# Optimization experiments

Measured on AMD Instinct MI355X. Metric: run time of the kernel, lower is better.

Reference implementation:

```python
import jax, jax.numpy as jnp
import numpy as np

EPS = 1e-6

def rms_norm(x, w):
    xf = x.astype(jnp.float32)
    xf = xf * jax.lax.rsqrt(jnp.mean(jnp.square(xf), axis=-1, keepdims=True) + EPS)
    return xf.astype(x.dtype) * w

def rotate_pairs(x):
    x = x.reshape(*x.shape[:-1], -1, 2)
    x1, x2 = x[..., 0], x[..., 1]
    return jnp.stack((-x2, x1), axis=-1).reshape(*x.shape[:-2], -1)

def apply_rope_axis(x, coords, inv_freq):
    # x: [B, H, T, axis_width]; coords: [T]; inv_freq: [axis_dim]
    angles = coords[:, None].astype(jnp.float32) * inv_freq[None, :]  # [T, axis_dim]
    cos = jnp.repeat(jnp.cos(angles), 2, axis=-1).astype(x.dtype)  # [T, axis_width]
    sin = jnp.repeat(jnp.sin(angles), 2, axis=-1).astype(x.dtype)
    return x * cos[None, None] + rotate_pairs(x) * sin[None, None]

def modulate(x, shift, scale):
    return x * (1.0 + scale[:, None, :]) + shift[:, None, :]

def setup_inputs() -> dict:
    key = jax.random.key(0)
    ks = jax.random.split(key, 16)
    B, T, D = 2, 2048, 1024
    HD = 64            # head_dim
    HID = 4096         # swiglu hidden (dim * mlp_ratio)
    CD = 1024          # cond_dim
    s = lambda n: 1.0 / np.sqrt(n)
    return {
        "x": jax.random.normal(ks[0], (B, T, D), jnp.float32),
        "cond": jax.random.normal(ks[1], (B, CD), jnp.float32),
        "norm1_w": jnp.ones((D,), jnp.float32),
        "qkv_w": jax.random.normal(ks[2], (3 * D, D), jnp.float32) * s(D),
        "q_norm_w": jnp.ones((HD,), jnp.float32),
        "k_norm_w": jnp.ones((HD,), jnp.float32),
        "proj_w": jax.random.normal(ks[3], (D, D), jnp.float32) * s(D),
        "proj_b": jnp.zeros((D,), jnp.float32),
        "norm2_w": jnp.ones((D,), jnp.float32),
        "fc1_w": jax.random.normal(ks[4], (2 * HID, D), jnp.float32) * s(D),
        "fc1_b": jnp.zeros((2 * HID,), jnp.float32),
        "fc2_w": jax.random.normal(ks[5], (D, HID), jnp.float32) * s(HID),
        "fc2_b": jnp.zeros((D,), jnp.float32),
        "ada_w": jax.random.normal(ks[6], (6 * D, CD), jnp.float32) * 0.02,
        "ada_b": jnp.zeros((6 * D,), jnp.float32),
        "height": 64,
        "width": 32,
    }

def reference(x, cond, norm1_w, qkv_w, q_norm_w, k_norm_w, proj_w, proj_b,
              norm2_w, fc1_w, fc1_b, fc2_w, fc2_b, ada_w, ada_b, height, width):
    B, T, D = x.shape
    HD = q_norm_w.shape[0]
    NH = D // HD
    scale = HD ** -0.5
    axis_dim = HD // 4
    axis_w = axis_dim * 2
    inv_freq = 1.0 / (10000.0 ** (jnp.arange(axis_dim, dtype=jnp.float32) / axis_dim))

    # AdaLN-Zero conditioning
    ada = jax.nn.silu(cond) @ ada_w.T + ada_b  # [B, 6D]
    sh_a, sc_a, g_a, sh_m, sc_m, g_m = jnp.split(ada, 6, axis=-1)

    # --- attention branch ---
    residual = x
    h = modulate(rms_norm(x, norm1_w), sh_a, sc_a)
    qkv = (h @ qkv_w.T).reshape(B, T, 3, NH, HD)
    q, k, v = qkv[:, :, 0], qkv[:, :, 1], qkv[:, :, 2]  # [B, T, NH, HD]
    q = rms_norm(q, q_norm_w)
    k = rms_norm(k, k_norm_w)
    q = q.transpose(0, 2, 1, 3)  # [B, NH, T, HD]
    k = k.transpose(0, 2, 1, 3)
    v = v.transpose(0, 2, 1, 3)

    # 2D RoPE: y coords on first axis_w dims, x coords on next axis_w dims
    yy, xx = jnp.meshgrid(jnp.arange(height), jnp.arange(width), indexing="ij")
    yy, xx = yy.reshape(-1), xx.reshape(-1)  # [T]
    q = jnp.concatenate([
        apply_rope_axis(q[..., :axis_w], yy, inv_freq),
        apply_rope_axis(q[..., axis_w:2 * axis_w], xx, inv_freq),
        q[..., 2 * axis_w:]], axis=-1)
    k = jnp.concatenate([
        apply_rope_axis(k[..., :axis_w], yy, inv_freq),
        apply_rope_axis(k[..., axis_w:2 * axis_w], xx, inv_freq),
        k[..., 2 * axis_w:]], axis=-1)

    attn = jax.nn.softmax(jnp.einsum("bhqd,bhkd->bhqk", q, k) * scale, axis=-1)
    h = jnp.einsum("bhqk,bhkd->bhqd", attn, v).transpose(0, 2, 1, 3).reshape(B, T, D)
    h = h @ proj_w.T + proj_b
    x = residual + g_a[:, None, :] * h

    # --- SwiGLU MLP branch ---
    residual = x
    h = modulate(rms_norm(x, norm2_w), sh_m, sc_m)
    value, gate = jnp.split(h @ fc1_w.T + fc1_b, 2, axis=-1)
    h = (value * jax.nn.silu(gate)) @ fc2_w.T + fc2_b
    return residual + g_m[:, None, :] * h
```

## Files before the change

kernel.cpp:

```cpp
#include <hip/hip_runtime.h>
#include <hip/hip_bf16.h>

#define B_   2
#define T_   2048
#define D_   1024
#define NH_  16
#define HD_  64
#define HID_ 4096
#define CD_  1024
#define SIX_D (6*D_)

typedef __bf16 bf16x8 __attribute__((ext_vector_type(8)));
typedef float  f32x4  __attribute__((ext_vector_type(4)));
typedef float  f32x16 __attribute__((ext_vector_type(16)));

__device__ __forceinline__ unsigned short f2bf(float f){
  union { float f; unsigned u; } v; v.f = f;
  unsigned r = v.u + 0x7FFFu + ((v.u >> 16) & 1u);
  return (unsigned short)(r >> 16);
}
__device__ __forceinline__ float bf2f(unsigned short u){
  union { unsigned x; float f; } v; v.x = ((unsigned)u) << 16; return v.f;
}

__device__ __forceinline__ void gl_lds16(const void* g, void* l){
  __builtin_amdgcn_global_load_lds(
      (__attribute__((address_space(1))) void*)const_cast<void*>(g),
      (__attribute__((address_space(3))) void*)l, 16, 0, 0);
}

__global__ void k_conv_all(const float* __restrict__ s0, const float* __restrict__ s1,
                           const float* __restrict__ s2, const float* __restrict__ s3,
                           unsigned short* __restrict__ d0, unsigned short* __restrict__ d1,
                           unsigned short* __restrict__ d2, unsigned short* __restrict__ d3){
  int bid = blockIdx.x;
  const float* s; unsigned short* d; int base;
  if (bid < 3072)      { s = s0; d = d0; base = bid; }
  else if (bid < 4096) { s = s1; d = d1; base = bid - 3072; }
  else if (bid < 12288){ s = s2; d = d2; base = bid - 4096; }
  else                 { s = s3; d = d3; base = bid - 12288; }
  int i = base*256 + threadIdx.x;
  float4 v = reinterpret_cast<const float4*>(s)[i];
  ushort4 o;
  o.x = f2bf(v.x); o.y = f2bf(v.y); o.z = f2bf(v.z); o.w = f2bf(v.w);
  reinterpret_cast<ushort4*>(d)[i] = o;
}

__global__ void k_ada(const float* __restrict__ cond, const float* __restrict__ ada_w,
                      const float* __restrict__ ada_b, float* __restrict__ ada){
  __shared__ float sc[CD_];
  __shared__ float part[4][64];
  int b = blockIdx.y;
  int tid = threadIdx.x;
  for (int i = tid; i < CD_; i += 256){
    float c = cond[b*CD_ + i];
    sc[i] = c / (1.f + __expf(-c));
  }
  __syncthreads();
  int col = blockIdx.x*64 + (tid & 63);
  int qk  = tid >> 6;
  const float* wr = ada_w + (size_t)col*CD_ + qk*256;
  const float* scq = sc + qk*256;
  float acc = 0.f;
  #pragma unroll 4
  for (int k = 0; k < 256; k++) acc += scq[k]*wr[k];
  part[qk][tid & 63] = acc;
  __syncthreads();
  if (tid < 64){
    float a = part[0][tid] + part[1][tid] + part[2][tid] + part[3][tid];
    int c = blockIdx.x*64 + tid;
    ada[b*SIX_D + c] = a + ada_b[c];
  }
}

__global__ void k_norm_mod(const float* __restrict__ x, const float* __restrict__ w,
                           const float* __restrict__ ada, int sh_off, int sc_off,
                           unsigned short* __restrict__ out){
  int row = blockIdx.x;
  int b = row >> 11;
  int tid = threadIdx.x;
  float4 xv = reinterpret_cast<const float4*>(x + (size_t)row*D_)[tid];
  float ss = xv.x*xv.x + xv.y*xv.y + xv.z*xv.z + xv.w*xv.w;
  #pragma unroll
  for (int m = 32; m > 0; m >>= 1) ss += __shfl_xor(ss, m, 64);
  __shared__ float red[4];
  int wave = tid >> 6;
  if ((tid & 63) == 0) red[wave] = ss;
  __syncthreads();
  float tot = red[0]+red[1]+red[2]+red[3];
  float rn = rsqrtf(tot * (1.f/(float)D_) + 1e-6f);
  float4 wv  = reinterpret_cast<const float4*>(w)[tid];
  float4 scv = reinterpret_cast<const float4*>(ada + b*SIX_D + sc_off)[tid];
  float4 shv = reinterpret_cast<const float4*>(ada + b*SIX_D + sh_off)[tid];
  ushort4 o;
  o.x = f2bf(xv.x*rn*wv.x*(1.f+scv.x)+shv.x);
  o.y = f2bf(xv.y*rn*wv.y*(1.f+scv.y)+shv.y);
  o.z = f2bf(xv.z*rn*wv.z*(1.f+scv.z)+shv.z);
  o.w = f2bf(xv.w*rn*wv.w*(1.f+scv.w)+shv.w);
  reinterpret_cast<ushort4*>(out + (size_t)row*D_)[tid] = o;
}

enum { EPI_F32 = 0, EPI_RESID = 1, EPI_BF16 = 2 };

template<int EPI>
__launch_bounds__(256)
__global__ void k_gemm_bt(const unsigned short* __restrict__ A,
                          const unsigned short* __restrict__ W,
                          int M, int N, int K,
                          void* __restrict__ outp,
                          const float* __restrict__ resid,
                          const float* __restrict__ ada, int g_off,
                          const float* __restrict__ bias){
  __shared__ __align__(16) unsigned short As[2][128*32];
  __shared__ __align__(16) unsigned short Bs[2][128*32];
  const int tid = threadIdx.x;
  const int wave = tid >> 6, lane = tid & 63;
  const int wm = (wave >> 1)*64, wn = (wave & 1)*64;
  const int m0 = blockIdx.y*128, n0 = blockIdx.x*128;
  const int fr = lane & 15, fq = lane >> 4;
  const int sl = (fq ^ ((fr >> 1) & 3))*8;
  const int r0 = tid >> 2, c0 = tid & 3;
  const int g0 = c0 ^ ((r0 >> 1) & 3);
  const int r1 = r0 + 64;
  const int g1 = c0 ^ ((r1 >> 1) & 3);
  const unsigned short* gA0 = A + (size_t)(m0 + r0)*K + g0*8;
  const unsigned short* gA1 = A + (size_t)(m0 + r1)*K + g1*8;
  const unsigned short* gB0 = W + (size_t)(n0 + r0)*K + g0*8;
  const unsigned short* gB1 = W + (size_t)(n0 + r1)*K + g1*8;
  const int l0 = (tid & ~63)*8, l1 = ((256 + tid) & ~63)*8;
  f32x4 acc[4][4] = {};
  auto stage = [&](int buf){
    gl_lds16(gA0, &As[buf][l0]);
    gl_lds16(gA1, &As[buf][l1]);
    gl_lds16(gB0, &Bs[buf][l0]);
    gl_lds16(gB1, &Bs[buf][l1]);
    gA0 += 32; gA1 += 32; gB0 += 32; gB1 += 32;
  };
  stage(0); stage(1);
  const int NK = K >> 5;
  for (int t = 0; t < NK; t++){
    const int cur = t & 1;
    if (t < NK - 1) asm volatile("s_waitcnt vmcnt(4)" ::: "memory");
    else            asm volatile("s_waitcnt vmcnt(0)" ::: "memory");
    __builtin_amdgcn_s_barrier();
    bf16x8 af[4], bfr[4];
    #pragma unroll
    for (int i = 0; i < 4; i++){
      af[i]  = *(const bf16x8*)&As[cur][(wm + i*16 + fr)*32 + sl];
      bfr[i] = *(const bf16x8*)&Bs[cur][(wn + i*16 + fr)*32 + sl];
    }
    __builtin_amdgcn_s_setprio(1);
    #pragma unroll
    for (int i = 0; i < 4; i++)
      #pragma unroll
      for (int j = 0; j < 4; j++)
        acc[i][j] = __builtin_amdgcn_mfma_f32_16x16x32_bf16(af[i], bfr[j], acc[i][j], 0,0,0);
    __builtin_amdgcn_s_setprio(0);
    __builtin_amdgcn_s_barrier();
    if (t + 2 < NK) stage(cur);
  }
  #pragma unroll
  for (int i = 0; i < 4; i++){
    #pragma unroll
    for (int j = 0; j < 4; j++){
      int col = n0 + wn + j*16 + fr;
      #pragma unroll
      for (int r = 0; r < 4; r++){
        int row = m0 + wm + i*16 + fq*4 + r;
        float v = acc[i][j][r];
        if (EPI == EPI_F32){
          ((float*)outp)[(size_t)row*N + col] = v;
        } else if (EPI == EPI_BF16){
          ((unsigned short*)outp)[(size_t)row*N + col] = f2bf(v);
        } else {
          int b = row >> 11;
          float g = ada[b*SIX_D + g_off + col];
          ((float*)outp)[(size_t)row*N + col] = resid[(size_t)row*N + col] + g*(v + bias[col]);
        }
      }
    }
  }
}

template<int EPI>
__launch_bounds__(256)
__global__ void k_gemm_bt64(const unsigned short* __restrict__ A,
                            const unsigned short* __restrict__ W,
                            int M, int N, int K,
                            void* __restrict__ outp,
                            const float* __restrict__ resid,
                            const float* __restrict__ ada, int g_off,
                            const float* __restrict__ bias){
  __shared__ __align__(16) unsigned short As[2][64*32];
  __shared__ __align__(16) unsigned short Bs[2][128*32];
  const int tid = threadIdx.x;
  const int wave = tid >> 6, lane = tid & 63;
  const int wm = (wave >> 1)*32, wn = (wave & 1)*64;
  const int m0 = blockIdx.y*64, n0 = blockIdx.x*128;
  const int fr = lane & 15, fq = lane >> 4;
  const int sl = (fq ^ ((fr >> 1) & 3))*8;
  const int r0 = tid >> 2, c0 = tid & 3;
  const int g0 = c0 ^ ((r0 >> 1) & 3);
  const int r1 = r0 + 64;
  const int g1 = c0 ^ ((r1 >> 1) & 3);
  const unsigned short* gA0 = A + (size_t)(m0 + r0)*K + g0*8;
  const unsigned short* gB0 = W + (size_t)(n0 + r0)*K + g0*8;
  const unsigned short* gB1 = W + (size_t)(n0 + r1)*K + g1*8;
  const int l0 = (tid & ~63)*8, l1 = ((256 + tid) & ~63)*8;
  f32x4 acc[2][4] = {};
  auto stage = [&](int buf){
    gl_lds16(gA0, &As[buf][l0]);
    gl_lds16(gB0, &Bs[buf][l0]);
    gl_lds16(gB1, &Bs[buf][l1]);
    gA0 += 32; gB0 += 32; gB1 += 32;
  };
  stage(0); stage(1);
  const int NK = K >> 5;
  for (int t = 0; t < NK; t++){
    const int cur = t & 1;
    if (t < NK - 1) asm volatile("s_waitcnt vmcnt(3)" ::: "memory");
    else            asm volatile("s_waitcnt vmcnt(0)" ::: "memory");
    __builtin_amdgcn_s_barrier();
    bf16x8 af[2], bfr[4];
    #pragma unroll
    for (int i = 0; i < 2; i++)
      af[i]  = *(const bf16x8*)&As[cur][(wm + i*16 + fr)*32 + sl];
    #pragma unroll
    for (int j = 0; j < 4; j++)
      bfr[j] = *(const bf16x8*)&Bs[cur][(wn + j*16 + fr)*32 + sl];
    __builtin_amdgcn_s_setprio(1);
    #pragma unroll
    for (int i = 0; i < 2; i++)
      #pragma unroll
      for (int j = 0; j < 4; j++)
        acc[i][j] = __builtin_amdgcn_mfma_f32_16x16x32_bf16(af[i], bfr[j], acc[i][j], 0,0,0);
    __builtin_amdgcn_s_setprio(0);
    __builtin_amdgcn_s_barrier();
    if (t + 2 < NK) stage(cur);
  }
  #pragma unroll
  for (int i = 0; i < 2; i++){
    #pragma unroll
    for (int j = 0; j < 4; j++){
      int col = n0 + wn + j*16 + fr;
      #pragma unroll
      for (int r = 0; r < 4; r++){
        int row = m0 + wm + i*16 + fq*4 + r;
        float v = acc[i][j][r];
        if (EPI == EPI_F32){
          ((float*)outp)[(size_t)row*N + col] = v;
        } else if (EPI == EPI_BF16){
          ((unsigned short*)outp)[(size_t)row*N + col] = f2bf(v);
        } else {
          int b = row >> 11;
          float g = ada[b*SIX_D + g_off + col];
          ((float*)outp)[(size_t)row*N + col] = resid[(size_t)row*N + col] + g*(v + bias[col]);
        }
      }
    }
  }
}

__launch_bounds__(256)
__global__ void k_gemm_fc1(const unsigned short* __restrict__ A,
                           const unsigned short* __restrict__ W,
                           const float* __restrict__ bias,
                           unsigned short* __restrict__ out){
  __shared__ __align__(16) unsigned short As[2][128*32];
  __shared__ __align__(16) unsigned short Bv[2][64*32];
  __shared__ __align__(16) unsigned short Bg[2][64*32];
  const int K = D_;
  const int tid = threadIdx.x;
  const int wave = tid >> 6, lane = tid & 63;
  const int wm = (wave >> 1)*64, wn = (wave & 1)*32;
  const int m0 = blockIdx.y*128, n0 = blockIdx.x*64;
  const int fr = lane & 15, fq = lane >> 4;
  const int sl = (fq ^ ((fr >> 1) & 3))*8;
  const int r0 = tid >> 2, c0 = tid & 3;
  const int g0 = c0 ^ ((r0 >> 1) & 3);
  const int r1 = r0 + 64;
  const int g1 = c0 ^ ((r1 >> 1) & 3);
  const unsigned short* gA0 = A + (size_t)(m0 + r0)*K + g0*8;
  const unsigned short* gA1 = A + (size_t)(m0 + r1)*K + g1*8;
  const unsigned short* gBv = W + (size_t)(n0 + r0)*K + g0*8;
  const unsigned short* gBg = W + (size_t)(HID_ + n0 + r0)*K + g0*8;
  const int l0 = (tid & ~63)*8, l1 = ((256 + tid) & ~63)*8;
  f32x4 accv[4][2] = {}, accg[4][2] = {};
  auto stage = [&](int buf){
    gl_lds16(gA0, &As[buf][l0]);
    gl_lds16(gA1, &As[buf][l1]);
    gl_lds16(gBv, &Bv[buf][l0]);
    gl_lds16(gBg, &Bg[buf][l0]);
    gA0 += 32; gA1 += 32; gBv += 32; gBg += 32;
  };
  stage(0); stage(1);
  const int NK = K >> 5;
  for (int t = 0; t < NK; t++){
    const int cur = t & 1;
    if (t < NK - 1) asm volatile("s_waitcnt vmcnt(4)" ::: "memory");
    else            asm volatile("s_waitcnt vmcnt(0)" ::: "memory");
    __builtin_amdgcn_s_barrier();
    bf16x8 af[4], bv[2], bg[2];
    #pragma unroll
    for (int i = 0; i < 4; i++)
      af[i] = *(const bf16x8*)&As[cur][(wm + i*16 + fr)*32 + sl];
    #pragma unroll
    for (int j = 0; j < 2; j++){
      bv[j] = *(const bf16x8*)&Bv[cur][(wn + j*16 + fr)*32 + sl];
      bg[j] = *(const bf16x8*)&Bg[cur][(wn + j*16 + fr)*32 + sl];
    }
    __builtin_amdgcn_s_setprio(1);
    #pragma unroll
    for (int i = 0; i < 4; i++)
      #pragma unroll
      for (int j = 0; j < 2; j++){
        accv[i][j] = __builtin_amdgcn_mfma_f32_16x16x32_bf16(af[i], bv[j], accv[i][j], 0,0,0);
        accg[i][j] = __builtin_amdgcn_mfma_f32_16x16x32_bf16(af[i], bg[j], accg[i][j], 0,0,0);
      }
    __builtin_amdgcn_s_setprio(0);
    __builtin_amdgcn_s_barrier();
    if (t + 2 < NK) stage(cur);
  }
  #pragma unroll
  for (int i = 0; i < 4; i++){
    #pragma unroll
    for (int j = 0; j < 2; j++){
      int col = n0 + wn + j*16 + fr;
      #pragma unroll
      for (int r = 0; r < 4; r++){
        int row = m0 + wm + i*16 + fq*4 + r;
        float vv = accv[i][j][r] + bias[col];
        float gg = accg[i][j][r] + bias[HID_ + col];
        float h = vv * (gg / (1.f + __expf(-gg)));
        out[(size_t)row*HID_ + col] = f2bf(h);
      }
    }
  }
}

__global__ void k_qkv_post(const unsigned short* __restrict__ qkv,
                           const float* __restrict__ qw, const float* __restrict__ kw,
                           const int* __restrict__ wptr,
                           unsigned short* __restrict__ q, unsigned short* __restrict__ k){
  int idx = blockIdx.x*4 + (threadIdx.x >> 6);
  int h = idx & (NH_-1);
  int t = (idx >> 4) & (T_-1);
  int b = idx >> 15;
  int d = threadIdx.x & 63;
  const unsigned short* base = qkv + (size_t)(b*T_ + t)*3072;
  float qv = bf2f(base[h*64 + d]);
  float kv = bf2f(base[1024 + h*64 + d]);
  float sq = qv*qv, sk = kv*kv;
  #pragma unroll
  for (int m = 32; m > 0; m >>= 1){ sq += __shfl_xor(sq, m, 64); sk += __shfl_xor(sk, m, 64); }
  qv *= rsqrtf(sq*(1.f/64.f) + 1e-6f) * qw[d];
  kv *= rsqrtf(sk*(1.f/64.f) + 1e-6f) * kw[d];
  int width = wptr[0];
  int yy = t / width, xx = t - yy*width;
  int coord = (d < 32) ? yy : xx;
  int fi = (d & 31) >> 1;
  float ifreq = __expf(-(float)fi * (9.210340371976184f/16.f));
  float ang = (float)coord * ifreq;
  float cs = cosf(ang), sn = sinf(ang);
  float pq = __shfl_xor(qv, 1, 64);
  float pk = __shfl_xor(kv, 1, 64);
  float rq = (d & 1) ? pq : -pq;
  float rk = (d & 1) ? pk : -pk;
  qv = qv*cs + rq*sn;
  kv = kv*cs + rk*sn;
  size_t o = ((size_t)(b*NH_ + h)*T_ + t)*64 + d;
  q[o] = f2bf(qv); k[o] = f2bf(kv);
}

__global__ void k_vtrans(const unsigned short* __restrict__ qkv, unsigned short* __restrict__ vt){
  __shared__ __align__(16) unsigned short TT[64*64];
  int bh = blockIdx.y, t0 = blockIdx.x*64;
  int b = bh >> 4, h = bh & 15;
  int tid = threadIdx.x;
  #pragma unroll
  for (int it = 0; it < 2; it++){
    int i2 = it*256 + tid;
    int t = i2 >> 3, c8 = (i2 & 7)*8;
    union { uint4 v; unsigned short u[8]; } ld;
    ld.v = *(const uint4*)(qkv + (size_t)(b*T_ + t0 + t)*3072 + 2048 + h*64 + c8);
    #pragma unroll
    for (int e = 0; e < 8; e++){
      int c = c8 + e;
      int gp = (t >> 3) ^ ((c >> 2) & 7);
      TT[c*64 + gp*8 + (t & 7)] = ld.u[e];
    }
  }
  __syncthreads();
  #pragma unroll
  for (int it = 0; it < 2; it++){
    int i2 = it*256 + tid;
    int d = i2 >> 3, g = i2 & 7;
    int gp = g ^ ((d >> 2) & 7);
    *(uint4*)(vt + ((size_t)(bh*64 + d)*T_ + t0 + g*8)) = *(const uint4*)&TT[d*64 + gp*8];
  }
}

__launch_bounds__(128, 2)
__global__ void k_attn(const unsigned short* __restrict__ q,
                       const unsigned short* __restrict__ k,
                       const unsigned short* __restrict__ vt,
                       unsigned short* __restrict__ out){
  __shared__ __align__(16) unsigned short Kl[2][64*64];
  __shared__ __align__(16) unsigned short Vl[2][64*64];
  const int tid  = threadIdx.x;
  const int wave = tid >> 6;
  const int lane = tid & 63;
  const int ln   = lane & 31;
  const int hi   = lane >> 5;
  const int id = blockIdx.x;
  const int bh = id & 31;
  const int q0 = (id >> 5)*64 + wave*32;

  bf16x8 qf[4];
  {
    const unsigned short* qp = q + ((size_t)bh*T_ + q0 + ln)*HD_ + hi*8;
    #pragma unroll
    for (int kk = 0; kk < 4; kk++)
      qf[kk] = *(const bf16x8*)(qp + kk*16);
  }
  const unsigned short* kg = k  + (size_t)bh*T_*HD_;
  const unsigned short* vg = vt + (size_t)bh*HD_*T_;

  auto stage = [&](int buf, int kt){
    #pragma unroll
    for (int rr = 0; rr < 4; rr++){
      int idx = rr*128 + tid;
      int row = idx >> 3, c = idx & 7;
      int g = c ^ (row & 7);
      gl_lds16(kg + (size_t)(kt + row)*HD_ + g*8, &Kl[buf][(idx & ~63)*8]);
      gl_lds16(vg + (size_t)row*T_ + kt + g*8,    &Vl[buf][(idx & ~63)*8]);
    }
  };

  f32x16 o0 = {}, o1 = {};
  float ls[4] = {};
  const int vr0 = ln*64, vr1 = (32 + ln)*64;
  const int sw = ln & 7;

  stage(0, 0);
  __syncthreads();

  for (int t = 0; t < T_/64; t++){
    const int cur = t & 1, nxt = cur ^ 1;
    if (t + 1 < T_/64) stage(nxt, (t + 1)*64);
    const unsigned short* Kc = Kl[cur];
    const unsigned short* Vc = Vl[cur];
    #pragma unroll
    for (int s2 = 0; s2 < 2; s2++){
      bf16x8 kf[4];
      const int kb = (s2*32 + ln)*64;
      #pragma unroll
      for (int kk = 0; kk < 4; kk++){
        int ch = (kk*2 + hi) ^ sw;
        kf[kk] = *(const bf16x8*)&Kc[kb + ch*8];
      }
      f32x16 sa = {}, sb = {};
      __builtin_amdgcn_s_setprio(1);
      sa = __builtin_amdgcn_mfma_f32_32x32x16_bf16(kf[0], qf[0], sa, 0, 0, 0);
      sb = __builtin_amdgcn_mfma_f32_32x32x16_bf16(kf[1], qf[1], sb, 0, 0, 0);
      sa = __builtin_amdgcn_mfma_f32_32x32x16_bf16(kf[2], qf[2], sa, 0, 0, 0);
      sb = __builtin_amdgcn_mfma_f32_32x32x16_bf16(kf[3], qf[3], sb, 0, 0, 0);
      __builtin_amdgcn_s_setprio(0);
      union { uint2 u2[2]; bf16x8 v; } v0f[2], v1f[2];
      #pragma unroll
      for (int c = 0; c < 2; c++){
        int chA = (s2*4 + c*2)     ^ sw;
        int chB = (s2*4 + c*2 + 1) ^ sw;
        v0f[c].u2[0] = *(const uint2*)&Vc[vr0 + chA*8 + hi*4];
        v0f[c].u2[1] = *(const uint2*)&Vc[vr0 + chB*8 + hi*4];
        v1f[c].u2[0] = *(const uint2*)&Vc[vr1 + chA*8 + hi*4];
        v1f[c].u2[1] = *(const uint2*)&Vc[vr1 + chB*8 + hi*4];
      }
      f32x16 sv = sa + sb;
      float p[16];
      #pragma unroll
      for (int r = 0; r < 16; r++)
        p[r] = __expf(fminf(sv[r]*0.125f, 30.f));
      union { __bf16 h[16]; bf16x8 v[2]; } pa;
      #pragma unroll
      for (int r = 0; r < 16; r++){
        pa.h[r] = (__bf16)p[r];
        ls[r & 3] += p[r];
      }
      __builtin_amdgcn_s_setprio(1);
      o0 = __builtin_amdgcn_mfma_f32_32x32x16_bf16(pa.v[0], v0f[0].v, o0, 0, 0, 0);
      o1 = __builtin_amdgcn_mfma_f32_32x32x16_bf16(pa.v[0], v1f[0].v, o1, 0, 0, 0);
      o0 = __builtin_amdgcn_mfma_f32_32x32x16_bf16(pa.v[1], v0f[1].v, o0, 0, 0, 0);
      o1 = __builtin_amdgcn_mfma_f32_32x32x16_bf16(pa.v[1], v1f[1].v, o1, 0, 0, 0);
      __builtin_amdgcn_s_setprio(0);
    }
    __syncthreads();
  }

  float lsum = ls[0] + ls[1] + ls[2] + ls[3];
  lsum += __shfl_xor(lsum, 32, 64);
  float inv = 1.f / lsum;
  const int b = bh >> 4, h = bh & 15;
  unsigned short* ob = out + ((size_t)(b*T_ + q0))*D_ + h*64 + ln;
  #pragma unroll
  for (int r = 0; r < 16; r++){
    int qr = (r & 3) + 8*(r >> 2) + 4*hi;
    float invr = __shfl(inv, qr, 64);
    unsigned short* op = ob + (size_t)qr*D_;
    op[0]  = f2bf(o0[r]*invr);
    op[32] = f2bf(o1[r]*invr);
  }
}

extern "C" void kernel_launch(void* const* d_in, const int* in_sizes, int n_in,
                              void* d_out, int out_size, void* d_ws, size_t ws_size,
                              hipStream_t stream){
  const float* x      = (const float*)d_in[0];
  const float* cond   = (const float*)d_in[1];
  const float* norm1w = (const float*)d_in[2];
  const float* qkv_w  = (const float*)d_in[3];
  const float* q_nw   = (const float*)d_in[4];
  const float* k_nw   = (const float*)d_in[5];
  const float* proj_w = (const float*)d_in[6];
  const float* proj_b = (const float*)d_in[7];
  const float* norm2w = (const float*)d_in[8];
  const float* fc1_w  = (const float*)d_in[9];
  const float* fc1_b  = (const float*)d_in[10];
  const float* fc2_w  = (const float*)d_in[11];
  const float* fc2_b  = (const float*)d_in[12];
  const float* ada_w  = (const float*)d_in[13];
  const float* ada_b  = (const float*)d_in[14];
  const int*   wptr   = (const int*)d_in[16];
  float* out = (float*)d_out;

  char* ws = (char*)d_ws;
  size_t off = 0;
  auto alloc = [&](size_t bytes)->void*{
    void* p = ws + off; off += (bytes + 255) & ~(size_t)255; return p;
  };
  unsigned short* w_qkv  = (unsigned short*)alloc(3072ull*1024*2);
  unsigned short* w_proj = (unsigned short*)alloc(1024ull*1024*2);
  unsigned short* w_fc1  = (unsigned short*)alloc(8192ull*1024*2);
  unsigned short* w_fc2  = (unsigned short*)alloc(1024ull*4096*2);
  float* ada             = (float*)alloc((size_t)B_*SIX_D*4);
  unsigned short* h1     = (unsigned short*)alloc(4096ull*1024*2);
  char* R                = (char*)alloc(4096ull*3072*4);
  unsigned short* qkv_out= (unsigned short*)R;
  unsigned short* attn_o = (unsigned short*)R;
  float* x1              = (float*)(R + (size_t)B_*T_*D_*2);
  unsigned short* qb     = (unsigned short*)alloc(32ull*2048*64*2);
  unsigned short* kb     = (unsigned short*)alloc(32ull*2048*64*2);
  unsigned short* vt     = (unsigned short*)alloc(32ull*64*2048*2);
  unsigned short* mlp    = (unsigned short*)alloc(4096ull*4096*2);
  (void)ws_size; (void)in_sizes; (void)n_in; (void)out_size;

  k_conv_all<<<16384, 256, 0, stream>>>(qkv_w, proj_w, fc1_w, fc2_w, w_qkv, w_proj, w_fc1, w_fc2);

  k_ada<<<dim3(SIX_D/64, B_), 256, 0, stream>>>(cond, ada_w, ada_b, ada);
  k_norm_mod<<<B_*T_, 256, 0, stream>>>(x, norm1w, ada, 0, D_, h1);
  k_gemm_bt<EPI_BF16><<<dim3(3072/128, 4096/128), 256, 0, stream>>>(
      h1, w_qkv, B_*T_, 3*D_, D_, qkv_out, nullptr, nullptr, 0, nullptr);
  k_qkv_post<<<B_*T_*NH_/4, 256, 0, stream>>>(qkv_out, q_nw, k_nw, wptr, qb, kb);
  k_vtrans<<<dim3(T_/64, 32), 256, 0, stream>>>(qkv_out, vt);
  k_attn<<<1024, 128, 0, stream>>>(qb, kb, vt, attn_o);
  k_gemm_bt64<EPI_RESID><<<dim3(1024/128, 4096/64), 256, 0, stream>>>(
      attn_o, w_proj, B_*T_, D_, D_, x1, x, ada, 2*D_, proj_b);
  k_norm_mod<<<B_*T_, 256, 0, stream>>>(x1, norm2w, ada, 3*D_, 4*D_, h1);
  k_gemm_fc1<<<dim3(HID_/64, 4096/128), 256, 0, stream>>>(h1, w_fc1, fc1_b, mlp);
  k_gemm_bt64<EPI_RESID><<<dim3(1024/128, 4096/64), 256, 0, stream>>>(
      mlp, w_fc2, B_*T_, D_, HID_, out, x1, ada, 5*D_, fc2_b);
}
```

Measured before the change: 472.7 us.

## Enlarge fc1 GEMM tile to 256 rows with 512 threads; coalesce ada GEMV

The fc1 SwiGLU GEMM block grows from 128x64 to 256x64 output rows using 8 waves. The value and gate weight tiles are loaded by separate halves of the block, so each weight tile is reused across twice as many rows and global B traffic per output drops. The adaLN GEMV is rewritten so each wave reduces 16 columns with lane-contiguous loads and a shuffle reduction, replacing strided per-thread row walks. The larger block uses more LDS and registers per block, which may lower occupancy or leave fewer blocks to spread across CUs.

```diff
diff --git a/kernel.cpp b/kernel.cpp
--- a/kernel.cpp
+++ b/kernel.cpp
@@ -49,7 +49,6 @@
 __global__ void k_ada(const float* __restrict__ cond, const float* __restrict__ ada_w,
                       const float* __restrict__ ada_b, float* __restrict__ ada){
   __shared__ float sc[CD_];
-  __shared__ float part[4][64];
   int b = blockIdx.y;
   int tid = threadIdx.x;
   for (int i = tid; i < CD_; i += 256){
@@ -57,19 +56,19 @@
     sc[i] = c / (1.f + __expf(-c));
   }
   __syncthreads();
-  int col = blockIdx.x*64 + (tid & 63);
-  int qk  = tid >> 6;
-  const float* wr = ada_w + (size_t)col*CD_ + qk*256;
-  const float* scq = sc + qk*256;
-  float acc = 0.f;
-  #pragma unroll 4
-  for (int k = 0; k < 256; k++) acc += scq[k]*wr[k];
-  part[qk][tid & 63] = acc;
-  __syncthreads();
-  if (tid < 64){
-    float a = part[0][tid] + part[1][tid] + part[2][tid] + part[3][tid];
-    int c = blockIdx.x*64 + tid;
-    ada[b*SIX_D + c] = a + ada_b[c];
+  int wave = tid >> 6, lane = tid & 63;
+  int colbase = blockIdx.x*64 + wave*16;
+  #pragma unroll
+  for (int c = 0; c < 16; c++){
+    int col = colbase + c;
+    const float* wr = ada_w + (size_t)col*CD_;
+    float acc = 0.f;
+    #pragma unroll
+    for (int i = 0; i < 16; i++)
+      acc += sc[lane + 64*i] * wr[lane + 64*i];
+    #pragma unroll
+    for (int m = 32; m > 0; m >>= 1) acc += __shfl_xor(acc, m, 64);
+    if (lane == 0) ada[b*SIX_D + col] = acc + ada_b[col];
   }
 }
 
@@ -261,53 +260,55 @@
   }
 }
 
-__launch_bounds__(256)
+__launch_bounds__(512)
 __global__ void k_gemm_fc1(const unsigned short* __restrict__ A,
                            const unsigned short* __restrict__ W,
                            const float* __restrict__ bias,
                            unsigned short* __restrict__ out){
-  __shared__ __align__(16) unsigned short As[2][128*32];
+  __shared__ __align__(16) unsigned short As[2][256*32];
   __shared__ __align__(16) unsigned short Bv[2][64*32];
   __shared__ __align__(16) unsigned short Bg[2][64*32];
   const int K = D_;
   const int tid = threadIdx.x;
   const int wave = tid >> 6, lane = tid & 63;
-  const int wm = (wave >> 1)*64, wn = (wave & 1)*32;
-  const int m0 = blockIdx.y*128, n0 = blockIdx.x*64;
+  const int wr = wave >> 1, wc = wave & 1;
+  const int m0 = blockIdx.y*256, n0 = blockIdx.x*64;
   const int fr = lane & 15, fq = lane >> 4;
   const int sl = (fq ^ ((fr >> 1) & 3))*8;
-  const int r0 = tid >> 2, c0 = tid & 3;
-  const int g0 = c0 ^ ((r0 >> 1) & 3);
-  const int r1 = r0 + 64;
-  const int g1 = c0 ^ ((r1 >> 1) & 3);
-  const unsigned short* gA0 = A + (size_t)(m0 + r0)*K + g0*8;
-  const unsigned short* gA1 = A + (size_t)(m0 + r1)*K + g1*8;
-  const unsigned short* gBv = W + (size_t)(n0 + r0)*K + g0*8;
-  const unsigned short* gBg = W + (size_t)(HID_ + n0 + r0)*K + g0*8;
-  const int l0 = (tid & ~63)*8, l1 = ((256 + tid) & ~63)*8;
+  const int ra0 = tid >> 2, ca = tid & 3;
+  const int ga0 = ca ^ ((ra0 >> 1) & 3);
+  const int ra1 = ra0 + 128;
+  const int ga1 = ca ^ ((ra1 >> 1) & 3);
+  const unsigned short* gA0 = A + (size_t)(m0 + ra0)*K + ga0*8;
+  const unsigned short* gA1 = A + (size_t)(m0 + ra1)*K + ga1*8;
+  const int la0 = (tid & ~63)*8, la1 = ((512 + tid) & ~63)*8;
+  const int tb = tid & 255;
+  const int rb = tb >> 2, cb = tb & 3;
+  const int gb = cb ^ ((rb >> 1) & 3);
+  const unsigned short* gB = W + (size_t)((tid < 256 ? 0 : HID_) + n0 + rb)*K + gb*8;
+  const int lb = (tb & ~63)*8;
   f32x4 accv[4][2] = {}, accg[4][2] = {};
   auto stage = [&](int buf){
-    gl_lds16(gA0, &As[buf][l0]);
-    gl_lds16(gA1, &As[buf][l1]);
-    gl_lds16(gBv, &Bv[buf][l0]);
-    gl_lds16(gBg, &Bg[buf][l0]);
-    gA0 += 32; gA1 += 32; gBv += 32; gBg += 32;
+    gl_lds16(gA0, &As[buf][la0]);
+    gl_lds16(gA1, &As[buf][la1]);
+    gl_lds16(gB, (tid < 256) ? &Bv[buf][lb] : &Bg[buf][lb]);
+    gA0 += 32; gA1 += 32; gB += 32;
   };
   stage(0); stage(1);
   const int NK = K >> 5;
   for (int t = 0; t < NK; t++){
     const int cur = t & 1;
-    if (t < NK - 1) asm volatile("s_waitcnt vmcnt(4)" ::: "memory");
+    if (t < NK - 1) asm volatile("s_waitcnt vmcnt(3)" ::: "memory");
     else            asm volatile("s_waitcnt vmcnt(0)" ::: "memory");
     __builtin_amdgcn_s_barrier();
     bf16x8 af[4], bv[2], bg[2];
     #pragma unroll
     for (int i = 0; i < 4; i++)
-      af[i] = *(const bf16x8*)&As[cur][(wm + i*16 + fr)*32 + sl];
+      af[i] = *(const bf16x8*)&As[cur][(wr*64 + i*16 + fr)*32 + sl];
     #pragma unroll
     for (int j = 0; j < 2; j++){
-      bv[j] = *(const bf16x8*)&Bv[cur][(wn + j*16 + fr)*32 + sl];
-      bg[j] = *(const bf16x8*)&Bg[cur][(wn + j*16 + fr)*32 + sl];
+      bv[j] = *(const bf16x8*)&Bv[cur][(wc*32 + j*16 + fr)*32 + sl];
+      bg[j] = *(const bf16x8*)&Bg[cur][(wc*32 + j*16 + fr)*32 + sl];
     }
     __builtin_amdgcn_s_setprio(1);
     #pragma unroll
@@ -325,10 +326,10 @@
   for (int i = 0; i < 4; i++){
     #pragma unroll
     for (int j = 0; j < 2; j++){
-      int col = n0 + wn + j*16 + fr;
+      int col = n0 + wc*32 + j*16 + fr;
       #pragma unroll
       for (int r = 0; r < 4; r++){
-        int row = m0 + wm + i*16 + fq*4 + r;
+        int row = m0 + wr*64 + i*16 + fq*4 + r;
         float vv = accv[i][j][r] + bias[col];
         float gg = accg[i][j][r] + bias[HID_ + col];
         float h = vv * (gg / (1.f + __expf(-gg)));
@@ -566,7 +567,7 @@
   k_gemm_bt64<EPI_RESID><<<dim3(1024/128, 4096/64), 256, 0, stream>>>(
       attn_o, w_proj, B_*T_, D_, D_, x1, x, ada, 2*D_, proj_b);
   k_norm_mod<<<B_*T_, 256, 0, stream>>>(x1, norm2w, ada, 3*D_, 4*D_, h1);
-  k_gemm_fc1<<<dim3(HID_/64, 4096/128), 256, 0, stream>>>(h1, w_fc1, fc1_b, mlp);
+  k_gemm_fc1<<<dim3(HID_/64, B_*T_/256), 512, 0, stream>>>(h1, w_fc1, fc1_b, mlp);
   k_gemm_bt64<EPI_RESID><<<dim3(1024/128, 4096/64), 256, 0, stream>>>(
       mlp, w_fc2, B_*T_, D_, HID_, out, x1, ada, 5*D_, fc2_b);
 }
```

Measured after the change: 495.0 us. 1.05x slower.

## Triple-buffer GEMM LDS staging and restructure adaLN projection per-wave

Applied to the files above, without the earlier changes.

Both bf16 GEMM kernels move from double to triple-buffered LDS staging, keeping two tiles of global loads in flight with vmcnt waits adjusted to match. This is meant to hide more global-memory latency behind the MFMA work. The extra LDS buffer raises shared memory per block, which may cut occupancy. Separately, the adaLN projection kernel now has each wave compute 16 columns with coalesced lane-strided weight reads and a shuffle reduction, replacing per-thread strided row reads and a shared-memory reduction.

```diff
diff --git a/kernel.cpp b/kernel.cpp
--- a/kernel.cpp
+++ b/kernel.cpp
@@ -49,7 +49,6 @@
 __global__ void k_ada(const float* __restrict__ cond, const float* __restrict__ ada_w,
                       const float* __restrict__ ada_b, float* __restrict__ ada){
   __shared__ float sc[CD_];
-  __shared__ float part[4][64];
   int b = blockIdx.y;
   int tid = threadIdx.x;
   for (int i = tid; i < CD_; i += 256){
@@ -57,19 +56,19 @@
     sc[i] = c / (1.f + __expf(-c));
   }
   __syncthreads();
-  int col = blockIdx.x*64 + (tid & 63);
-  int qk  = tid >> 6;
-  const float* wr = ada_w + (size_t)col*CD_ + qk*256;
-  const float* scq = sc + qk*256;
-  float acc = 0.f;
-  #pragma unroll 4
-  for (int k = 0; k < 256; k++) acc += scq[k]*wr[k];
-  part[qk][tid & 63] = acc;
-  __syncthreads();
-  if (tid < 64){
-    float a = part[0][tid] + part[1][tid] + part[2][tid] + part[3][tid];
-    int c = blockIdx.x*64 + tid;
-    ada[b*SIX_D + c] = a + ada_b[c];
+  int wave = tid >> 6, lane = tid & 63;
+  int colbase = blockIdx.x*64 + wave*16;
+  #pragma unroll
+  for (int c = 0; c < 16; c++){
+    int col = colbase + c;
+    const float* wr = ada_w + (size_t)col*CD_;
+    float acc = 0.f;
+    #pragma unroll
+    for (int i = 0; i < 16; i++)
+      acc += sc[lane + 64*i] * wr[lane + 64*i];
+    #pragma unroll
+    for (int m = 32; m > 0; m >>= 1) acc += __shfl_xor(acc, m, 64);
+    if (lane == 0) ada[b*SIX_D + col] = acc + ada_b[col];
   }
 }
 
@@ -111,8 +110,8 @@
                           const float* __restrict__ resid,
                           const float* __restrict__ ada, int g_off,
                           const float* __restrict__ bias){
-  __shared__ __align__(16) unsigned short As[2][128*32];
-  __shared__ __align__(16) unsigned short Bs[2][128*32];
+  __shared__ __align__(16) unsigned short As[3][128*32];
+  __shared__ __align__(16) unsigned short Bs[3][128*32];
   const int tid = threadIdx.x;
   const int wave = tid >> 6, lane = tid & 63;
   const int wm = (wave >> 1)*64, wn = (wave & 1)*64;
@@ -136,12 +135,13 @@
     gl_lds16(gB1, &Bs[buf][l1]);
     gA0 += 32; gA1 += 32; gB0 += 32; gB1 += 32;
   };
-  stage(0); stage(1);
+  stage(0); stage(1); stage(2);
   const int NK = K >> 5;
+  int cur = 0;
   for (int t = 0; t < NK; t++){
-    const int cur = t & 1;
-    if (t < NK - 1) asm volatile("s_waitcnt vmcnt(4)" ::: "memory");
-    else            asm volatile("s_waitcnt vmcnt(0)" ::: "memory");
+    if (t < NK - 2)      asm volatile("s_waitcnt vmcnt(8)" ::: "memory");
+    else if (t < NK - 1) asm volatile("s_waitcnt vmcnt(4)" ::: "memory");
+    else                 asm volatile("s_waitcnt vmcnt(0)" ::: "memory");
     __builtin_amdgcn_s_barrier();
     bf16x8 af[4], bfr[4];
     #pragma unroll
@@ -157,7 +157,8 @@
         acc[i][j] = __builtin_amdgcn_mfma_f32_16x16x32_bf16(af[i], bfr[j], acc[i][j], 0,0,0);
     __builtin_amdgcn_s_setprio(0);
     __builtin_amdgcn_s_barrier();
-    if (t + 2 < NK) stage(cur);
+    if (t + 3 < NK) stage(cur);
+    cur = (cur == 2) ? 0 : cur + 1;
   }
   #pragma unroll
   for (int i = 0; i < 4; i++){
@@ -191,8 +192,8 @@
                             const float* __restrict__ resid,
                             const float* __restrict__ ada, int g_off,
                             const float* __restrict__ bias){
-  __shared__ __align__(16) unsigned short As[2][64*32];
-  __shared__ __align__(16) unsigned short Bs[2][128*32];
+  __shared__ __align__(16) unsigned short As[3][64*32];
+  __shared__ __align__(16) unsigned short Bs[3][128*32];
   const int tid = threadIdx.x;
   const int wave = tid >> 6, lane = tid & 63;
   const int wm = (wave >> 1)*32, wn = (wave & 1)*64;
@@ -214,12 +215,13 @@
     gl_lds16(gB1, &Bs[buf][l1]);
     gA0 += 32; gB0 += 32; gB1 += 32;
   };
-  stage(0); stage(1);
+  stage(0); stage(1); stage(2);
   const int NK = K >> 5;
+  int cur = 0;
   for (int t = 0; t < NK; t++){
-    const int cur = t & 1;
-    if (t < NK - 1) asm volatile("s_waitcnt vmcnt(3)" ::: "memory");
-    else            asm volatile("s_waitcnt vmcnt(0)" ::: "memory");
+    if (t < NK - 2)      asm volatile("s_waitcnt vmcnt(6)" ::: "memory");
+    else if (t < NK - 1) asm volatile("s_waitcnt vmcnt(3)" ::: "memory");
+    else                 asm volatile("s_waitcnt vmcnt(0)" ::: "memory");
     __builtin_amdgcn_s_barrier();
     bf16x8 af[2], bfr[4];
     #pragma unroll
@@ -236,7 +238,8 @@
         acc[i][j] = __builtin_amdgcn_mfma_f32_16x16x32_bf16(af[i], bfr[j], acc[i][j], 0,0,0);
     __builtin_amdgcn_s_setprio(0);
     __builtin_amdgcn_s_barrier();
-    if (t + 2 < NK) stage(cur);
+    if (t + 3 < NK) stage(cur);
+    cur = (cur == 2) ? 0 : cur + 1;
   }
   #pragma unroll
   for (int i = 0; i < 2; i++){
```

Result: no change. 465.0 us (-1.6%).
